# Optimization experiments

Hardware: AMD Instinct MI355X
Metric: run time of the kernel (lower is better)

## Reference

```python
import jax, jax.numpy as jnp
import numpy as np

EPS = 1e-6


def _cosine(mem, keys):
    # mem: [B,N,C], keys: [B,C,R] -> [B,N,R]
    dot = jnp.einsum('bnc,bcr->bnr', mem, keys)
    mn = jnp.linalg.norm(mem, axis=2, keepdims=True)      # [B,N,1]
    kn = jnp.linalg.norm(keys, axis=1, keepdims=True)     # [B,1,R]
    return dot / (mn * kn + EPS)


def setup_inputs() -> dict:
    B, N, C, R = 8, 2048, 256, 4
    key = jax.random.key(0)
    ks = jax.random.split(key, 16)
    return {
        'memory': jax.random.normal(ks[0], (B, N, C), jnp.float32),
        'link': jax.random.uniform(ks[1], (B, N, N), jnp.float32),
        'usage': jax.random.uniform(ks[2], (B, N), jnp.float32),
        'read_weights': jax.random.uniform(ks[3], (B, N, R), jnp.float32),
        'write_weight_prev': jax.random.uniform(ks[4], (B, N), jnp.float32),
        'precedence': jax.random.uniform(ks[5], (B, N), jnp.float32),
        'read_keys': jax.random.normal(ks[6], (B, C, R), jnp.float32),
        'read_strengths': jax.random.uniform(ks[7], (B, R), jnp.float32),
        'write_key': jax.random.normal(ks[8], (B, C), jnp.float32),
        'write_strength': jax.random.uniform(ks[9], (B, 1), jnp.float32),
        'free_gates': jax.random.uniform(ks[10], (B, R), jnp.float32),
        'allocation_gate': jax.random.uniform(ks[11], (B, 1), jnp.float32),
        'write_gate': jax.random.uniform(ks[12], (B, 1), jnp.float32),
        'write_vector': jax.random.normal(ks[13], (B, C), jnp.float32),
        'erase_vector': jax.random.uniform(ks[14], (B, C), jnp.float32),
        'read_modes': jax.random.uniform(ks[15], (B, 3, R), jnp.float32),
    }


def reference(memory, link, usage, read_weights, write_weight_prev, precedence,
              read_keys, read_strengths, write_key, write_strength, free_gates,
              allocation_gate, write_gate, write_vector, erase_vector, read_modes):
    B, N, C = memory.shape
    # --- usage update: psi retention from free gates ---
    psi = jnp.prod(1.0 - free_gates[:, None, :] * read_weights, axis=2)  # [B,N]
    u = (usage + write_weight_prev - usage * write_weight_prev) * psi
    # --- allocation weighting (sorted exclusive cumprod) ---
    order = jnp.argsort(u, axis=1)                                     # ascending usage
    u_sorted = jnp.take_along_axis(u, order, axis=1)
    excl = jnp.concatenate([jnp.ones_like(u_sorted[:, :1]),
                            jnp.cumprod(u_sorted[:, :-1], axis=1)], axis=1)
    a_sorted = (1.0 - u_sorted) * excl
    inv = jnp.argsort(order, axis=1)
    alloc = jnp.take_along_axis(a_sorted, inv, axis=1)                 # [B,N]
    # --- write weighting ---
    phi_w = _cosine(memory, write_key[:, :, None])[:, :, 0]            # [B,N]
    cw = jax.nn.softmax(phi_w * write_strength, axis=1)
    ww = write_gate * (allocation_gate * alloc + (1.0 - allocation_gate) * cw)  # [B,N]
    # --- memory write (erase + add) ---
    mem_new = memory * (1.0 - ww[:, :, None] * erase_vector[:, None, :]) \
              + ww[:, :, None] * write_vector[:, None, :]
    # --- precedence + link matrix ---
    prec_new = (1.0 - jnp.sum(ww, axis=1, keepdims=True)) * precedence + ww
    link_new = (1.0 - ww[:, :, None] - ww[:, None, :]) * link \
               + ww[:, :, None] * precedence[:, None, :]
    link_new = link_new * (1.0 - jnp.eye(N, dtype=link.dtype))[None]
    # --- directional weightings ---
    fwd = jnp.einsum('bij,bjr->bir', link_new, read_weights)           # [B,N,R]
    bwd = jnp.einsum('bji,bjr->bir', link_new, read_weights)
    # --- content read weighting on updated memory ---
    phi_r = _cosine(mem_new, read_keys)                                # [B,N,R]
    cr = jax.nn.softmax(phi_r * read_strengths[:, None, :], axis=1)
    rw_new = read_modes[:, 0][:, None, :] * bwd \
             + read_modes[:, 1][:, None, :] * cr \
             + read_modes[:, 2][:, None, :] * fwd                      # [B,N,R]
    # --- read vectors ---
    read_vectors = jnp.einsum('bnc,bnr->bcr', mem_new, rw_new)         # [B,C,R]
    return read_vectors
```

## Files before the change

### kernel.cpp

```cpp
#include <hip/hip_runtime.h>
#include <math.h>

#define EPS 1e-6f
constexpr int B = 8, N = 2048, C = 256, R = 4;

__device__ __forceinline__ float wred_sum(float v) {
  for (int d = 32; d; d >>= 1) v += __shfl_xor(v, d, 64);
  return v;
}

__device__ __forceinline__ float ww_inline(float sw, float al, float dw,
                                           float agv, float wgv) {
  return wgv * (agv * al + (1.f - agv) * (expf(sw) / dw));
}

__global__ __launch_bounds__(1024) void k_pre(const float* __restrict__ usage,
    const float* __restrict__ wwp, const float* __restrict__ fg,
    const float* __restrict__ rw, const float* __restrict__ mem,
    const float* __restrict__ wk, const float* __restrict__ wstr,
    float* __restrict__ alloc_, float* __restrict__ sw_, float* __restrict__ denw) {
  __shared__ float2 ulg[N];
  __shared__ float Sp[16][64];
  __shared__ float eacc[16];
  int blk = blockIdx.x;
  int t = threadIdx.x;
  if (blk < 256) {
    int b = blk >> 5, chunk = blk & 31;
    float gx = fg[b * R + 0], gy = fg[b * R + 1], gz = fg[b * R + 2], gw2 = fg[b * R + 3];
    for (int e = t; e < N; e += 1024) {
      float4 r4 = *(const float4*)&rw[(size_t)(b * N + e) * R];
      float psi = (1.f - gx * r4.x) * (1.f - gy * r4.y) * (1.f - gz * r4.z) * (1.f - gw2 * r4.w);
      float us = usage[b * N + e], w = wwp[b * N + e];
      float u = (us + w - us * w) * psi;
      ulg[e] = make_float2(u, log2f(u));
    }
    __syncthreads();
    int i = chunk * 64 + (t & 63);
    int jseg = t >> 6;
    float ui = ulg[i].x;
    float S = 0.f;
    int j0 = jseg * 128;
    #pragma unroll 4
    for (int jj = 0; jj < 128; jj++) {
      int j = j0 + jj;
      float2 v = ulg[j];
      bool sel = (v.x < ui) || (v.x == ui && j < i);
      S += sel ? v.y : 0.f;
    }
    Sp[jseg][t & 63] = S;
    __syncthreads();
    if (t < 64) {
      float tot = 0.f;
      #pragma unroll
      for (int s = 0; s < 16; s++) tot += Sp[s][t];
      int ii = chunk * 64 + t;
      alloc_[b * N + ii] = (1.f - ulg[ii].x) * exp2f(tot);
    }
  } else {
    int wv = t >> 6, lane = t & 63;
    int gw = (blk - 256) * 16 + wv;
    int b = gw >> 11, n = gw & (N - 1);
    float4 m4 = *(const float4*)&mem[(size_t)(b * N + n) * C + lane * 4];
    float4 k4 = *(const float4*)&wk[b * C + lane * 4];
    float dot = m4.x * k4.x + m4.y * k4.y + m4.z * k4.z + m4.w * k4.w;
    float nrm = m4.x * m4.x + m4.y * m4.y + m4.z * m4.z + m4.w * m4.w;
    float knr = k4.x * k4.x + k4.y * k4.y + k4.z * k4.z + k4.w * k4.w;
    for (int d = 32; d; d >>= 1) {
      dot += __shfl_xor(dot, d, 64);
      nrm += __shfl_xor(nrm, d, 64);
      knr += __shfl_xor(knr, d, 64);
    }
    if (lane == 0) {
      float phi = dot / (sqrtf(nrm) * sqrtf(knr) + EPS);
      float swv = phi * wstr[b];
      sw_[b * N + n] = swv;
      eacc[wv] = expf(swv);
    }
    __syncthreads();
    if (t == 0) {
      float s = 0.f;
      #pragma unroll
      for (int i = 0; i < 16; i++) s += eacc[i];
      atomicAdd(&denw[b], s);
    }
  }
}

__global__ __launch_bounds__(512, 4) void k_mid(const float* __restrict__ link,
    const float* __restrict__ rw, const float* __restrict__ sw_,
    const float* __restrict__ alloc_, const float* __restrict__ denw,
    const float* __restrict__ ag, const float* __restrict__ wg,
    const float* __restrict__ prec, const float* __restrict__ mem,
    const float* __restrict__ rk, const float* __restrict__ ev,
    const float* __restrict__ wvec, const float* __restrict__ rs,
    float* __restrict__ t_, float* __restrict__ upart, float* __restrict__ sr_,
    float* __restrict__ denr, float* __restrict__ ST_) {
  __shared__ float tred[32][8][8];
  __shared__ float ri8[32][8];
  __shared__ float eacc[8][4];
  __shared__ float red8[8][8];
  const int blk = blockIdx.x;
  const int t = threadIdx.x;
  const int lane = t & 63, wv = t >> 6;
  if (blk < 512) {
    const int b = blk >> 6;
    const int strip = blk & 63;
    const int i0 = strip * 32;
    const int jb = t * 4;
    const float agv = ag[b], wgv = wg[b], dw = denw[b];
    if (t < 32) {
      int i = i0 + t;
      float4 q = *(const float4*)&rw[(size_t)(b * N + i) * R];
      float wi = ww_inline(sw_[b * N + i], alloc_[b * N + i], dw, agv, wgv);
      ri8[t][0] = q.x; ri8[t][1] = q.y; ri8[t][2] = q.z; ri8[t][3] = q.w;
      ri8[t][4] = wi * q.x; ri8[t][5] = wi * q.y; ri8[t][6] = wi * q.z; ri8[t][7] = wi * q.w;
    }
    float cw[4][8];
    {
      float4 sw4 = *(const float4*)&sw_[b * N + jb];
      float4 al4 = *(const float4*)&alloc_[b * N + jb];
      float wj[4] = { ww_inline(sw4.x, al4.x, dw, agv, wgv),
                      ww_inline(sw4.y, al4.y, dw, agv, wgv),
                      ww_inline(sw4.z, al4.z, dw, agv, wgv),
                      ww_inline(sw4.w, al4.w, dw, agv, wgv) };
      #pragma unroll
      for (int k = 0; k < 4; k++) {
        float4 r4 = *(const float4*)&rw[(size_t)(b * N + jb + k) * R];
        cw[k][0] = r4.x; cw[k][1] = r4.y; cw[k][2] = r4.z; cw[k][3] = r4.w;
        cw[k][4] = wj[k] * r4.x; cw[k][5] = wj[k] * r4.y;
        cw[k][6] = wj[k] * r4.z; cw[k][7] = wj[k] * r4.w;
      }
    }
    float uacc[4][8];
    #pragma unroll
    for (int k = 0; k < 4; k++) {
      #pragma unroll
      for (int r = 0; r < 8; r++) uacc[k][r] = 0.f;
    }
    __syncthreads();
    const float* Lbase = link + (size_t)(b * N + i0) * N;
    for (int ii = 0; ii < 32; ii += 2) {
      float4 La[2];
      La[0] = *(const float4*)(Lbase + (size_t)(ii + 0) * N + jb);
      La[1] = *(const float4*)(Lbase + (size_t)(ii + 1) * N + jb);
      float trow[2][8];
      #pragma unroll
      for (int p = 0; p < 2; p++) {
        float lv[4] = { La[p].x, La[p].y, La[p].z, La[p].w };
        float ri[8];
        #pragma unroll
        for (int r = 0; r < 8; r++) { ri[r] = ri8[ii + p][r]; trow[p][r] = 0.f; }
        #pragma unroll
        for (int k = 0; k < 4; k++) {
          #pragma unroll
          for (int r = 0; r < 8; r++) {
            uacc[k][r] = fmaf(lv[k], ri[r], uacc[k][r]);
            trow[p][r] = fmaf(lv[k], cw[k][r], trow[p][r]);
          }
        }
      }
      float nv[2][4];
      #pragma unroll
      for (int p = 0; p < 2; p++) {
        #pragma unroll
        for (int rr = 0; rr < 4; rr++) {
          float a = trow[p][2 * rr], c = trow[p][2 * rr + 1];
          float oa = __shfl_xor(a, 1, 64), oc = __shfl_xor(c, 1, 64);
          nv[p][rr] = (lane & 1) ? (c + oc) : (a + oa);
        }
      }
      float nw[2][2];
      #pragma unroll
      for (int p = 0; p < 2; p++) {
        #pragma unroll
        for (int rr = 0; rr < 2; rr++) {
          float a = nv[p][2 * rr], c = nv[p][2 * rr + 1];
          float oa = __shfl_xor(a, 2, 64), oc = __shfl_xor(c, 2, 64);
          nw[p][rr] = (lane & 2) ? (c + oc) : (a + oa);
        }
      }
      float vv[2];
      #pragma unroll
      for (int p = 0; p < 2; p++) {
        float a2 = nw[p][0], c2 = nw[p][1];
        float oa2 = __shfl_xor(a2, 4, 64), oc2 = __shfl_xor(c2, 4, 64);
        vv[p] = (lane & 4) ? (c2 + oc2) : (a2 + oa2);
      }
      #pragma unroll
      for (int p = 0; p < 2; p++) vv[p] += __shfl_xor(vv[p], 8, 64);
      #pragma unroll
      for (int p = 0; p < 2; p++) vv[p] += __shfl_xor(vv[p], 16, 64);
      #pragma unroll
      for (int p = 0; p < 2; p++) vv[p] += __shfl_xor(vv[p], 32, 64);
      if (lane < 8) {
        tred[ii + 0][wv][lane] = vv[0];
        tred[ii + 1][wv][lane] = vv[1];
      }
    }
    __syncthreads();
    if (t < 256) {
      int i = t >> 3, r = t & 7;
      float s = 0.f;
      #pragma unroll
      for (int w8 = 0; w8 < 8; w8++) s += tred[i][w8][r];
      t_[((size_t)(b * 8 + r)) * N + i0 + i] = s;
    }
    float* ub = upart + ((size_t)(b * 64 + strip) * 8) * N;
    #pragma unroll
    for (int r = 0; r < 8; r++) {
      float4 v = { uacc[0][r], uacc[1][r], uacc[2][r], uacc[3][r] };
      *(float4*)(ub + (size_t)r * N + jb) = v;
    }
  } else if (blk < 2560) {
    int gw = (blk - 512) * 8 + wv;
    int b = gw >> 11, n = gw & (N - 1);
    const float agv = ag[b], wgv = wg[b], dw = denw[b];
    float w = ww_inline(sw_[b * N + n], alloc_[b * N + n], dw, agv, wgv);
    int c0 = lane * 4;
    float4 m4 = *(const float4*)&mem[(size_t)(b * N + n) * C + c0];
    float4 e4 = *(const float4*)&ev[b * C + c0];
    float4 v4 = *(const float4*)&wvec[b * C + c0];
    float mn[4] = { m4.x * (1.f - w * e4.x) + w * v4.x,
                    m4.y * (1.f - w * e4.y) + w * v4.y,
                    m4.z * (1.f - w * e4.z) + w * v4.z,
                    m4.w * (1.f - w * e4.w) + w * v4.w };
    float dot[4] = { 0, 0, 0, 0 };
    float kn[4] = { 0, 0, 0, 0 };
    float nrm = 0.f;
    #pragma unroll
    for (int ci = 0; ci < 4; ci++) {
      float4 k4 = *(const float4*)&rk[(size_t)(b * C + c0 + ci) * R];
      dot[0] = fmaf(mn[ci], k4.x, dot[0]);
      dot[1] = fmaf(mn[ci], k4.y, dot[1]);
      dot[2] = fmaf(mn[ci], k4.z, dot[2]);
      dot[3] = fmaf(mn[ci], k4.w, dot[3]);
      kn[0] = fmaf(k4.x, k4.x, kn[0]);
      kn[1] = fmaf(k4.y, k4.y, kn[1]);
      kn[2] = fmaf(k4.z, k4.z, kn[2]);
      kn[3] = fmaf(k4.w, k4.w, kn[3]);
      nrm = fmaf(mn[ci], mn[ci], nrm);
    }
    for (int d = 32; d; d >>= 1) {
      dot[0] += __shfl_xor(dot[0], d, 64);
      dot[1] += __shfl_xor(dot[1], d, 64);
      dot[2] += __shfl_xor(dot[2], d, 64);
      dot[3] += __shfl_xor(dot[3], d, 64);
      kn[0] += __shfl_xor(kn[0], d, 64);
      kn[1] += __shfl_xor(kn[1], d, 64);
      kn[2] += __shfl_xor(kn[2], d, 64);
      kn[3] += __shfl_xor(kn[3], d, 64);
      nrm += __shfl_xor(nrm, d, 64);
    }
    if (lane == 0) {
      float mnorm = sqrtf(nrm);
      #pragma unroll
      for (int r = 0; r < 4; r++) {
        float phi = dot[r] / (mnorm * sqrtf(kn[r]) + EPS);
        float sv = phi * rs[b * R + r];
        sr_[(size_t)(b * R + r) * N + n] = sv;
        eacc[wv][r] = expf(sv);
      }
    }
    __syncthreads();
    if (t < 4) {
      float s = 0.f;
      #pragma unroll
      for (int i = 0; i < 8; i++) s += eacc[i][t];
      atomicAdd(&denr[b * R + t], s);
    }
  } else {
    int b = blk - 2560;
    const float agv = ag[b], wgv = wg[b], dw = denw[b];
    float a[8] = { 0, 0, 0, 0, 0, 0, 0, 0 };
    #pragma unroll
    for (int k = 0; k < 4; k++) {
      int i = t + k * 512;
      float4 r4 = *(const float4*)&rw[(size_t)(b * N + i) * R];
      float pc = prec[b * N + i];
      float w = ww_inline(sw_[b * N + i], alloc_[b * N + i], dw, agv, wgv);
      a[0] = fmaf(pc, r4.x, a[0]); a[1] = fmaf(pc, r4.y, a[1]);
      a[2] = fmaf(pc, r4.z, a[2]); a[3] = fmaf(pc, r4.w, a[3]);
      a[4] = fmaf(w, r4.x, a[4]);  a[5] = fmaf(w, r4.y, a[5]);
      a[6] = fmaf(w, r4.z, a[6]);  a[7] = fmaf(w, r4.w, a[7]);
    }
    #pragma unroll
    for (int r = 0; r < 8; r++) a[r] = wred_sum(a[r]);
    if (lane == 0) {
      #pragma unroll
      for (int r = 0; r < 8; r++) red8[wv][r] = a[r];
    }
    __syncthreads();
    if (t < 8) {
      float s = 0.f;
      #pragma unroll
      for (int i = 0; i < 8; i++) s += red8[i][t];
      ST_[b * 8 + t] = s;
    }
  }
}

__global__ __launch_bounds__(256) void k_combread(const float* __restrict__ link,
    const float* __restrict__ sw_, const float* __restrict__ alloc_,
    const float* __restrict__ denw, const float* __restrict__ denr,
    const float* __restrict__ ag, const float* __restrict__ wg,
    const float* __restrict__ prec, const float* __restrict__ rw,
    const float* __restrict__ t_, const float* __restrict__ upart,
    const float* __restrict__ sr_, const float* __restrict__ ST_,
    const float* __restrict__ modes, const float* __restrict__ mem,
    const float* __restrict__ ev, const float* __restrict__ wvec,
    float* __restrict__ part_) {
  __shared__ float dgl[64], wloc[64], rwnl[4][64];
  __shared__ float red[4][64][4][4];
  const int blk = blockIdx.x;
  const int b = blk >> 5, chunk = blk & 31;
  const int n0 = chunk * 64;
  const int t = threadIdx.x;
  const int nl = t & 63, r = t >> 6;
  const int n = n0 + nl;
  const float agv = ag[b], wgv = wg[b], dw = denw[b];
  float u1 = 0.f, u2 = 0.f;
  const float* up = upart + ((size_t)(b * 64) * 8) * N;
  #pragma unroll 8
  for (int s = 0; s < 64; s++) {
    const float* p = up + ((size_t)s * 8) * N;
    u1 += p[(size_t)r * N + n];
    u2 += p[(size_t)(4 + r) * N + n];
  }
  float pc = prec[b * N + n];
  if (r == 0) {
    float w = ww_inline(sw_[b * N + n], alloc_[b * N + n], dw, agv, wgv);
    float L = link[((size_t)(b * N + n)) * N + n];
    dgl[nl] = (1.f - 2.f * w) * L + w * pc;
    wloc[nl] = w;
  }
  __syncthreads();
  {
    float w = wloc[nl], Dg = dgl[nl];
    float t1 = t_[(size_t)(b * 8 + r) * N + n];
    float t2 = t_[(size_t)(b * 8 + 4 + r) * N + n];
    float sv = sr_[(size_t)(b * R + r) * N + n];
    float cr = expf(sv) / denr[b * R + r];
    float rv = rw[(size_t)(b * N + n) * R + r];
    float S = ST_[b * 8 + r], T = ST_[b * 8 + 4 + r];
    float m0 = modes[(b * 3 + 0) * R + r], m1 = modes[(b * 3 + 1) * R + r],
          m2 = modes[(b * 3 + 2) * R + r];
    float fwd = (1.f - w) * t1 - t2 + w * S - Dg * rv;
    float bwd = (1.f - w) * u1 - u2 + pc * T - Dg * rv;
    rwnl[r][nl] = m0 * bwd + m1 * cr + m2 * fwd;
  }
  __syncthreads();
  const int sub = r, cg = nl;
  const int c0 = cg * 4;
  float4 e4 = *(const float4*)&ev[b * C + c0];
  float4 v4 = *(const float4*)&wvec[b * C + c0];
  float acc[4][4];
  #pragma unroll
  for (int ci = 0; ci < 4; ci++) {
    #pragma unroll
    for (int rr = 0; rr < 4; rr++) acc[ci][rr] = 0.f;
  }
  for (int m = 0; m < 16; m++) {
    int row = sub * 16 + m;
    int nn = n0 + row;
    float w = wloc[row];
    float4 m4 = *(const float4*)&mem[(size_t)(b * N + nn) * C + c0];
    float mn[4] = { m4.x * (1.f - w * e4.x) + w * v4.x,
                    m4.y * (1.f - w * e4.y) + w * v4.y,
                    m4.z * (1.f - w * e4.z) + w * v4.z,
                    m4.w * (1.f - w * e4.w) + w * v4.w };
    float rv[4] = { rwnl[0][row], rwnl[1][row], rwnl[2][row], rwnl[3][row] };
    #pragma unroll
    for (int ci = 0; ci < 4; ci++) {
      #pragma unroll
      for (int rr = 0; rr < 4; rr++) acc[ci][rr] = fmaf(mn[ci], rv[rr], acc[ci][rr]);
    }
  }
  #pragma unroll
  for (int ci = 0; ci < 4; ci++) {
    #pragma unroll
    for (int rr = 0; rr < 4; rr++) red[sub][cg][ci][rr] = acc[ci][rr];
  }
  __syncthreads();
  if (sub == 0) {
    #pragma unroll
    for (int ci = 0; ci < 4; ci++) {
      #pragma unroll
      for (int rr = 0; rr < 4; rr++) {
        float s = red[0][cg][ci][rr] + red[1][cg][ci][rr] +
                  red[2][cg][ci][rr] + red[3][cg][ci][rr];
        part_[((size_t)blk * C + (c0 + ci)) * R + rr] = s;
      }
    }
  }
}

__global__ void k_final(const float* __restrict__ part_, float* __restrict__ out) {
  int idx = blockIdx.x * 256 + threadIdx.x;
  if (idx >= B * C * R) return;
  int b = idx / (C * R), cr = idx % (C * R);
  float s = 0.f;
  for (int ch = 0; ch < 32; ch++) s += part_[(size_t)(b * 32 + ch) * C * R + cr];
  out[idx] = s;
}

extern "C" void kernel_launch(void* const* d_in, const int* in_sizes, int n_in,
                              void* d_out, int out_size, void* d_ws, size_t ws_size,
                              hipStream_t stream) {
  const float* mem   = (const float*)d_in[0];
  const float* link  = (const float*)d_in[1];
  const float* usage = (const float*)d_in[2];
  const float* rw    = (const float*)d_in[3];
  const float* wwp   = (const float*)d_in[4];
  const float* prec  = (const float*)d_in[5];
  const float* rk    = (const float*)d_in[6];
  const float* rs    = (const float*)d_in[7];
  const float* wk    = (const float*)d_in[8];
  const float* wstr  = (const float*)d_in[9];
  const float* fg    = (const float*)d_in[10];
  const float* ag    = (const float*)d_in[11];
  const float* wg    = (const float*)d_in[12];
  const float* wvec  = (const float*)d_in[13];
  const float* ev    = (const float*)d_in[14];
  const float* modes = (const float*)d_in[15];
  float* out = (float*)d_out;

  float* W = (float*)d_ws;
  float* denw  = W;
  float* denr  = W + 8;
  float* alloc_= W + 64;
  float* sw_   = alloc_ + B * N;
  float* ST_   = sw_ + B * N;
  float* t_    = ST_ + 64;
  float* sr_   = t_ + B * 8 * N;
  float* part_ = sr_ + B * R * N;
  float* upart = part_ + B * 32 * C * R;

  (void)hipMemsetAsync(W, 0, 64 * sizeof(float), stream);
  k_pre<<<256 + (B * N) / 16, 1024, 0, stream>>>(usage, wwp, fg, rw, mem, wk, wstr,
                                                 alloc_, sw_, denw);
  k_mid<<<512 + (B * N) / 8 + B, 512, 0, stream>>>(link, rw, sw_, alloc_, denw, ag, wg,
                                                   prec, mem, rk, ev, wvec, rs,
                                                   t_, upart, sr_, denr, ST_);
  k_combread<<<B * 32, 256, 0, stream>>>(link, sw_, alloc_, denw, denr, ag, wg, prec,
                                         rw, t_, upart, sr_, ST_, modes, mem, ev,
                                         wvec, part_);
  k_final<<<(B * C * R) / 256, 256, 0, stream>>>(part_, out);
}
```

Before: 136.0 us.

## Retile link pass to 64-row strips split into column halves

The link-matrix pass in k_mid now gives each block 64 rows and half the columns, with two columns per thread, instead of 32 rows across all columns with four per thread. This halves the number of partial column sums written to upart and read back in k_combread. The row-sum output becomes two partial buffers that k_combread adds together. Loads narrow from float4 to float2, and the min-blocks-per-CU hint is dropped, which may change register allocation and occupancy.

```diff
diff --git a/kernel.cpp b/kernel.cpp
--- a/kernel.cpp
+++ b/kernel.cpp
@@ -86,17 +86,17 @@
   }
 }
 
-__global__ __launch_bounds__(512, 4) void k_mid(const float* __restrict__ link,
+__global__ __launch_bounds__(512) void k_mid(const float* __restrict__ link,
     const float* __restrict__ rw, const float* __restrict__ sw_,
     const float* __restrict__ alloc_, const float* __restrict__ denw,
     const float* __restrict__ ag, const float* __restrict__ wg,
     const float* __restrict__ prec, const float* __restrict__ mem,
     const float* __restrict__ rk, const float* __restrict__ ev,
     const float* __restrict__ wvec, const float* __restrict__ rs,
-    float* __restrict__ t_, float* __restrict__ upart, float* __restrict__ sr_,
+    float* __restrict__ tpart, float* __restrict__ upart, float* __restrict__ sr_,
     float* __restrict__ denr, float* __restrict__ ST_) {
-  __shared__ float tred[32][8][8];
-  __shared__ float ri8[32][8];
+  __shared__ float tred[64][8][8];
+  __shared__ float ri8[64][8];
   __shared__ float eacc[8][4];
   __shared__ float red8[8][8];
   const int blk = blockIdx.x;
@@ -104,54 +104,53 @@
   const int lane = t & 63, wv = t >> 6;
   if (blk < 512) {
     const int b = blk >> 6;
-    const int strip = blk & 63;
-    const int i0 = strip * 32;
-    const int jb = t * 4;
+    const int strip = (blk >> 1) & 31;
+    const int half = blk & 1;
+    const int i0 = strip * 64;
+    const int jb = half * 1024 + t * 2;
     const float agv = ag[b], wgv = wg[b], dw = denw[b];
-    if (t < 32) {
+    if (t < 64) {
       int i = i0 + t;
       float4 q = *(const float4*)&rw[(size_t)(b * N + i) * R];
       float wi = ww_inline(sw_[b * N + i], alloc_[b * N + i], dw, agv, wgv);
       ri8[t][0] = q.x; ri8[t][1] = q.y; ri8[t][2] = q.z; ri8[t][3] = q.w;
       ri8[t][4] = wi * q.x; ri8[t][5] = wi * q.y; ri8[t][6] = wi * q.z; ri8[t][7] = wi * q.w;
     }
-    float cw[4][8];
+    float cw[2][8];
     {
-      float4 sw4 = *(const float4*)&sw_[b * N + jb];
-      float4 al4 = *(const float4*)&alloc_[b * N + jb];
-      float wj[4] = { ww_inline(sw4.x, al4.x, dw, agv, wgv),
-                      ww_inline(sw4.y, al4.y, dw, agv, wgv),
-                      ww_inline(sw4.z, al4.z, dw, agv, wgv),
-                      ww_inline(sw4.w, al4.w, dw, agv, wgv) };
-      #pragma unroll
-      for (int k = 0; k < 4; k++) {
+      float2 sw2 = *(const float2*)&sw_[b * N + jb];
+      float2 al2 = *(const float2*)&alloc_[b * N + jb];
+      float wj[2] = { ww_inline(sw2.x, al2.x, dw, agv, wgv),
+                      ww_inline(sw2.y, al2.y, dw, agv, wgv) };
+      #pragma unroll
+      for (int k = 0; k < 2; k++) {
         float4 r4 = *(const float4*)&rw[(size_t)(b * N + jb + k) * R];
         cw[k][0] = r4.x; cw[k][1] = r4.y; cw[k][2] = r4.z; cw[k][3] = r4.w;
         cw[k][4] = wj[k] * r4.x; cw[k][5] = wj[k] * r4.y;
         cw[k][6] = wj[k] * r4.z; cw[k][7] = wj[k] * r4.w;
       }
     }
-    float uacc[4][8];
-    #pragma unroll
-    for (int k = 0; k < 4; k++) {
+    float uacc[2][8];
+    #pragma unroll
+    for (int k = 0; k < 2; k++) {
       #pragma unroll
       for (int r = 0; r < 8; r++) uacc[k][r] = 0.f;
     }
     __syncthreads();
     const float* Lbase = link + (size_t)(b * N + i0) * N;
-    for (int ii = 0; ii < 32; ii += 2) {
-      float4 La[2];
-      La[0] = *(const float4*)(Lbase + (size_t)(ii + 0) * N + jb);
-      La[1] = *(const float4*)(Lbase + (size_t)(ii + 1) * N + jb);
+    for (int ii = 0; ii < 64; ii += 2) {
+      float2 La[2];
+      La[0] = *(const float2*)(Lbase + (size_t)(ii + 0) * N + jb);
+      La[1] = *(const float2*)(Lbase + (size_t)(ii + 1) * N + jb);
       float trow[2][8];
       #pragma unroll
       for (int p = 0; p < 2; p++) {
-        float lv[4] = { La[p].x, La[p].y, La[p].z, La[p].w };
+        float lv[2] = { La[p].x, La[p].y };
         float ri[8];
         #pragma unroll
         for (int r = 0; r < 8; r++) { ri[r] = ri8[ii + p][r]; trow[p][r] = 0.f; }
         #pragma unroll
-        for (int k = 0; k < 4; k++) {
+        for (int k = 0; k < 2; k++) {
           #pragma unroll
           for (int r = 0; r < 8; r++) {
             uacc[k][r] = fmaf(lv[k], ri[r], uacc[k][r]);
@@ -198,18 +197,18 @@
       }
     }
     __syncthreads();
-    if (t < 256) {
+    {
       int i = t >> 3, r = t & 7;
       float s = 0.f;
       #pragma unroll
       for (int w8 = 0; w8 < 8; w8++) s += tred[i][w8][r];
-      t_[((size_t)(b * 8 + r)) * N + i0 + i] = s;
-    }
-    float* ub = upart + ((size_t)(b * 64 + strip) * 8) * N;
+      tpart[((size_t)((b * 2 + half) * 8 + r)) * N + i0 + i] = s;
+    }
+    float* ub = upart + ((size_t)(b * 32 + strip) * 8) * N;
     #pragma unroll
     for (int r = 0; r < 8; r++) {
-      float4 v = { uacc[0][r], uacc[1][r], uacc[2][r], uacc[3][r] };
-      *(float4*)(ub + (size_t)r * N + jb) = v;
+      float2 v = { uacc[0][r], uacc[1][r] };
+      *(float2*)(ub + (size_t)r * N + jb) = v;
     }
   } else if (blk < 2560) {
     int gw = (blk - 512) * 8 + wv;
@@ -304,7 +303,7 @@
     const float* __restrict__ denw, const float* __restrict__ denr,
     const float* __restrict__ ag, const float* __restrict__ wg,
     const float* __restrict__ prec, const float* __restrict__ rw,
-    const float* __restrict__ t_, const float* __restrict__ upart,
+    const float* __restrict__ tpart, const float* __restrict__ upart,
     const float* __restrict__ sr_, const float* __restrict__ ST_,
     const float* __restrict__ modes, const float* __restrict__ mem,
     const float* __restrict__ ev, const float* __restrict__ wvec,
@@ -319,9 +318,9 @@
   const int n = n0 + nl;
   const float agv = ag[b], wgv = wg[b], dw = denw[b];
   float u1 = 0.f, u2 = 0.f;
-  const float* up = upart + ((size_t)(b * 64) * 8) * N;
+  const float* up = upart + ((size_t)(b * 32) * 8) * N;
   #pragma unroll 8
-  for (int s = 0; s < 64; s++) {
+  for (int s = 0; s < 32; s++) {
     const float* p = up + ((size_t)s * 8) * N;
     u1 += p[(size_t)r * N + n];
     u2 += p[(size_t)(4 + r) * N + n];
@@ -336,8 +335,10 @@
   __syncthreads();
   {
     float w = wloc[nl], Dg = dgl[nl];
-    float t1 = t_[(size_t)(b * 8 + r) * N + n];
-    float t2 = t_[(size_t)(b * 8 + 4 + r) * N + n];
+    float t1 = tpart[(size_t)((b * 2 + 0) * 8 + r) * N + n] +
+               tpart[(size_t)((b * 2 + 1) * 8 + r) * N + n];
+    float t2 = tpart[(size_t)((b * 2 + 0) * 8 + 4 + r) * N + n] +
+               tpart[(size_t)((b * 2 + 1) * 8 + 4 + r) * N + n];
     float sv = sr_[(size_t)(b * R + r) * N + n];
     float cr = expf(sv) / denr[b * R + r];
     float rv = rw[(size_t)(b * N + n) * R + r];
@@ -430,8 +431,8 @@
   float* alloc_= W + 64;
   float* sw_   = alloc_ + B * N;
   float* ST_   = sw_ + B * N;
-  float* t_    = ST_ + 64;
-  float* sr_   = t_ + B * 8 * N;
+  float* tpart = ST_ + 64;
+  float* sr_   = tpart + B * 16 * N;
   float* part_ = sr_ + B * R * N;
   float* upart = part_ + B * 32 * C * R;
 
@@ -440,9 +441,9 @@
                                                  alloc_, sw_, denw);
   k_mid<<<512 + (B * N) / 8 + B, 512, 0, stream>>>(link, rw, sw_, alloc_, denw, ag, wg,
                                                    prec, mem, rk, ev, wvec, rs,
-                                                   t_, upart, sr_, denr, ST_);
+                                                   tpart, upart, sr_, denr, ST_);
   k_combread<<<B * 32, 256, 0, stream>>>(link, sw_, alloc_, denw, denr, ag, wg, prec,
-                                         rw, t_, upart, sr_, ST_, modes, mem, ev,
+                                         rw, tpart, upart, sr_, ST_, modes, mem, ev,
                                          wvec, part_);
   k_final<<<(B * C * R) / 256, 256, 0, stream>>>(part_, out);
 }
```

New measurement: 150.9 us. +10.9%, slower.
